# Kernel optimization log

Hardware: AMD Instinct MI355X
Metric: run time of the kernel (lower is better)

Reference implementation:

```python
import jax, jax.numpy as jnp
import numpy as np

EMBED = 1024
HEADS = 16
DEPTH = EMBED // HEADS
FFN_DIM = 4096
EPS = 1e-9


def layer_norm(x, g, b):
    mu = jnp.mean(x, axis=-1, keepdims=True)
    var = jnp.mean(jnp.square(x - mu), axis=-1, keepdims=True)
    return (x - mu) * jax.lax.rsqrt(var + EPS) * g + b


def setup_inputs() -> dict:
    key = jax.random.key(0)
    ks = jax.random.split(key, 16)
    B, S = 2, 2048
    s_e = 1.0 / np.sqrt(EMBED)
    s_f = 1.0 / np.sqrt(FFN_DIM)
    return {
        "x": jax.random.normal(ks[0], (B, S, EMBED), dtype=jnp.float32),
        "mask": jnp.zeros((B, 1, 1, S), dtype=jnp.float32),
        "wq_w": jax.random.normal(ks[1], (EMBED, EMBED), dtype=jnp.float32) * s_e,
        "wq_b": jnp.zeros((EMBED,), dtype=jnp.float32),
        "wk_w": jax.random.normal(ks[2], (EMBED, EMBED), dtype=jnp.float32) * s_e,
        "wk_b": jnp.zeros((EMBED,), dtype=jnp.float32),
        "wv_w": jax.random.normal(ks[3], (EMBED, EMBED), dtype=jnp.float32) * s_e,
        "wv_b": jnp.zeros((EMBED,), dtype=jnp.float32),
        "wo_w": jax.random.normal(ks[4], (EMBED, EMBED), dtype=jnp.float32) * s_e,
        "wo_b": jnp.zeros((EMBED,), dtype=jnp.float32),
        "f1_w": jax.random.normal(ks[5], (EMBED, FFN_DIM), dtype=jnp.float32) * s_e,
        "f1_b": jnp.zeros((FFN_DIM,), dtype=jnp.float32),
        "f2_w": jax.random.normal(ks[6], (FFN_DIM, EMBED), dtype=jnp.float32) * s_f,
        "f2_b": jnp.zeros((EMBED,), dtype=jnp.float32),
        "ln1_g": jnp.ones((EMBED,), dtype=jnp.float32),
        "ln1_b": jnp.zeros((EMBED,), dtype=jnp.float32),
        "ln2_g": jnp.ones((EMBED,), dtype=jnp.float32),
        "ln2_b": jnp.zeros((EMBED,), dtype=jnp.float32),
    }


def reference(x, mask, wq_w, wq_b, wk_w, wk_b, wv_w, wv_b, wo_w, wo_b,
              f1_w, f1_b, f2_w, f2_b, ln1_g, ln1_b, ln2_g, ln2_b):
    B, S, E = x.shape

    def split_heads(t):  # (B,S,E) -> (B,H,S,D)
        return t.reshape(B, S, HEADS, DEPTH).transpose(0, 2, 1, 3)

    q = split_heads(x @ wq_w + wq_b)
    k = split_heads(x @ wk_w + wk_b)
    v = split_heads(x @ wv_w + wv_b)

    logits = jnp.einsum("bhqd,bhkd->bhqk", q, k) / jnp.sqrt(jnp.float32(DEPTH))
    logits = logits + mask * -1e12  # mask broadcast (B,1,1,S)
    attn = jax.nn.softmax(logits, axis=-1)
    out = jnp.einsum("bhqk,bhkd->bhqd", attn, v)
    out = out.transpose(0, 2, 1, 3).reshape(B, S, E)
    out = out @ wo_w + wo_b

    # dropout is identity (is_train=False)
    h = layer_norm(out + x, ln1_g, ln1_b)
    f = jax.nn.relu(h @ f1_w + f1_b) @ f2_w + f2_b
    return layer_norm(f + h, ln2_g, ln2_b)
```

## Files before the change

kernel.cpp:

```cpp
#include <hip/hip_runtime.h>
#include <hip/hip_bf16.h>
#include <stdint.h>

typedef __hip_bfloat16 bf16;
typedef __attribute__((ext_vector_type(8))) short short8;
typedef __attribute__((ext_vector_type(4))) short short4v;
typedef __attribute__((ext_vector_type(4))) float floatx4;

#define E_DIM 1024
#define S_LEN 2048
#define NB    2
#define NH    16
#define HD    64
#define FFN   4096
#define MTOT  4096

__device__ __forceinline__ void gl_lds16(const void* g, void* l) {
  __builtin_amdgcn_global_load_lds(
      (__attribute__((address_space(1))) void*)(g),
      (__attribute__((address_space(3))) void*)(l), 16, 0, 0);
}

__device__ __forceinline__ int fswz_v(int row) { return row & 7; }
__device__ __forceinline__ int fswz_k(int row) {
  return ((row ^ (row >> 3)) & 3) | ((((row >> 3) ^ (row >> 4)) & 1) << 2);
}

__global__ __launch_bounds__(256)
void cvt_bf16(const float* __restrict__ in, bf16* __restrict__ out) {
  const size_t i = ((size_t)blockIdx.x * 256 + threadIdx.x) * 4;
  float4 v = *(const float4*)(in + i);
  out[i + 0] = __float2bfloat16(v.x);
  out[i + 1] = __float2bfloat16(v.y);
  out[i + 2] = __float2bfloat16(v.z);
  out[i + 3] = __float2bfloat16(v.w);
}

__global__ __launch_bounds__(256)
void transpose4(const float* __restrict__ s0, const float* __restrict__ s1,
                const float* __restrict__ s2, const float* __restrict__ s3,
                bf16* __restrict__ d0, bf16* __restrict__ d1,
                bf16* __restrict__ d2, bf16* __restrict__ d3) {
  const int z = blockIdx.z;
  const float* in = (z == 0) ? s0 : (z == 1) ? s1 : (z == 2) ? s2 : s3;
  bf16* out = (z == 0) ? d0 : (z == 1) ? d1 : (z == 2) ? d2 : d3;
  __shared__ float tile[32][33];
  const int tx = threadIdx.x & 31;
  const int ty = threadIdx.x >> 5;
  const int c0 = blockIdx.x * 32;
  const int r0 = blockIdx.y * 32;
#pragma unroll
  for (int j = 0; j < 32; j += 8)
    tile[ty + j][tx] = in[(size_t)(r0 + ty + j) * 1024 + c0 + tx];
  __syncthreads();
#pragma unroll
  for (int j = 0; j < 32; j += 8)
    out[(size_t)(c0 + ty + j) * 1024 + r0 + tx] = __float2bfloat16(tile[tx][ty + j]);
}

__global__ __launch_bounds__(256)
void transpose_cvt(const float* __restrict__ in, bf16* __restrict__ out,
                   int R, int C) {
  __shared__ float tile[32][33];
  const int tx = threadIdx.x & 31;
  const int ty = threadIdx.x >> 5;
  const int c0 = blockIdx.x * 32;
  const int r0 = blockIdx.y * 32;
#pragma unroll
  for (int j = 0; j < 32; j += 8)
    tile[ty + j][tx] = in[(size_t)(r0 + ty + j) * C + c0 + tx];
  __syncthreads();
#pragma unroll
  for (int j = 0; j < 32; j += 8)
    out[(size_t)(c0 + ty + j) * R + r0 + tx] = __float2bfloat16(tile[tx][ty + j]);
}

__global__ __launch_bounds__(256)
void prep_bias(const float* __restrict__ qb, const float* __restrict__ kb,
               const float* __restrict__ vb, float* __restrict__ out) {
  const int i = blockIdx.x * 256 + threadIdx.x;
  float v = (i < 1024) ? qb[i] * 0.125f
                       : ((i < 2048) ? kb[i - 1024] : vb[i - 2048]);
  out[i] = v;
}

__global__ __launch_bounds__(256)
void gemm_bt(const bf16* __restrict__ A, const bf16* __restrict__ B,
             const float* __restrict__ bias, void* __restrict__ Cout,
             int M, int N, int K, int mode) {
  __shared__ alignas(16) bf16 sA[128 * 32];
  __shared__ alignas(16) bf16 sB[128 * 32];
  const int tid   = threadIdx.x;
  const int wave  = tid >> 6;
  const int lane  = tid & 63;
  const int row16 = lane & 15;
  const int quad  = lane >> 4;
  const int m0 = blockIdx.x * 128;
  const int n0 = blockIdx.y * 128;
  const int wm = (wave >> 1) * 64;
  const int wn = (wave & 1) * 64;

  floatx4 acc[4][4];
#pragma unroll
  for (int i = 0; i < 4; i++)
#pragma unroll
    for (int j = 0; j < 4; j++) {
      floatx4 z = {0.f, 0.f, 0.f, 0.f};
      acc[i][j] = z;
    }

  for (int k0 = 0; k0 < K; k0 += 32) {
#pragma unroll
    for (int j = 0; j < 2; ++j) {
      const int chunk = wave * 2 + j;
      const int e = chunk * 512 + lane * 8;
      const int r = e >> 5;
      const int kk = e & 31;
      gl_lds16(A + (size_t)(m0 + r) * K + k0 + kk, sA + chunk * 512);
      gl_lds16(B + (size_t)(n0 + r) * K + k0 + kk, sB + chunk * 512);
    }
    __syncthreads();

    short8 af[4], bfr[4];
#pragma unroll
    for (int i = 0; i < 4; i++) {
      af[i]  = *(const short8*)(sA + (wm + i * 16 + row16) * 32 + quad * 8);
      bfr[i] = *(const short8*)(sB + (wn + i * 16 + row16) * 32 + quad * 8);
    }
#pragma unroll
    for (int mi = 0; mi < 4; mi++)
#pragma unroll
      for (int ni = 0; ni < 4; ni++)
        acc[mi][ni] = __builtin_amdgcn_mfma_f32_16x16x32_bf16(
            af[mi], bfr[ni], acc[mi][ni], 0, 0, 0);
    __syncthreads();
  }

  float bval[4];
#pragma unroll
  for (int ni = 0; ni < 4; ni++) bval[ni] = bias[n0 + wn + ni * 16 + row16];

#pragma unroll
  for (int mi = 0; mi < 4; mi++) {
#pragma unroll
    for (int ni = 0; ni < 4; ni++) {
      const int col = n0 + wn + ni * 16 + row16;
      if (mode == 0) {
#pragma unroll
        for (int r = 0; r < 4; r++) {
          const int row = m0 + wm + mi * 16 + quad * 4 + r;
          ((float*)Cout)[(size_t)row * N + col] = acc[mi][ni][r] + bval[ni];
        }
      } else if (mode == 1) {
#pragma unroll
        for (int r = 0; r < 4; r++) {
          const int row = m0 + wm + mi * 16 + quad * 4 + r;
          float v = acc[mi][ni][r] + bval[ni];
          v = v > 0.f ? v : 0.f;
          ((bf16*)Cout)[(size_t)row * N + col] = __float2bfloat16(v);
        }
      } else {
        const int mat = col >> 10;
        const int c10 = col & 1023;
        const int hh = c10 >> 6, dd = c10 & 63;
        const float scl = (mat == 0) ? 0.125f : 1.0f;
        bf16* qout = (bf16*)Cout;
        const int rbase = m0 + wm + mi * 16 + quad * 4;
        const int b = rbase >> 11, s = rbase & 2047;
        const size_t bh = (size_t)b * NH + hh;
        if (mat == 2) {
          bf16* vt = qout + (1 << 23);
          short4v pv;
#pragma unroll
          for (int r = 0; r < 4; r++) {
            bf16 t = __float2bfloat16(acc[mi][ni][r] + bval[ni]);
            pv[r] = *(short*)&t;
          }
          *(short4v*)(vt + (bh * HD + dd) * S_LEN + s) = pv;
        } else {
          bf16* o = (mat == 1) ? (qout + (1 << 22)) : qout;
#pragma unroll
          for (int r = 0; r < 4; r++) {
            float v = acc[mi][ni][r] * scl + bval[ni];
            o[(bh * S_LEN + s + r) * HD + dd] = __float2bfloat16(v);
          }
        }
      }
    }
  }
}

__global__ __launch_bounds__(256, 4)
void flash_attn(const bf16* __restrict__ Q, const bf16* __restrict__ K,
                const bf16* __restrict__ Vt, const float* __restrict__ mask,
                bf16* __restrict__ Out) {
  __shared__ alignas(16) bf16 sK[64 * 64];
  __shared__ alignas(16) bf16 sV[64 * 64];
  __shared__ alignas(16) float sM[S_LEN];

  const int tid   = threadIdx.x;
  const int wave  = tid >> 6;
  const int lane  = tid & 63;
  const int row16 = lane & 15;
  const int quad  = lane >> 4;
  const int bh = blockIdx.y;
  const int b = bh >> 4, h = bh & 15;
  const int q0 = blockIdx.x * 64;
  const int qg = q0 + wave * 16 + row16;

  const bf16* qp = Q + ((size_t)bh * S_LEN + qg) * HD;
  short8 qf0 = *(const short8*)(qp + quad * 8);
  short8 qf1 = *(const short8*)(qp + 32 + quad * 8);

  for (int i = tid; i < S_LEN / 4; i += 256) {
    float4 mv = ((const float4*)(mask + (size_t)b * S_LEN))[i];
    float4 w = {-1e12f * mv.x, -1e12f * mv.y, -1e12f * mv.z, -1e12f * mv.w};
    ((float4*)sM)[i] = w;
  }

  float m_i = -1e30f, l_i = 0.f;
  floatx4 ov[4];
#pragma unroll
  for (int i = 0; i < 4; i++) { floatx4 z = {0.f,0.f,0.f,0.f}; ov[i] = z; }

  const bf16* Kbase = K + (size_t)bh * S_LEN * HD;
  const bf16* Vbase = Vt + (size_t)bh * HD * S_LEN;

  for (int kt = 0; kt < S_LEN / 64; ++kt) {
    const bf16* Kg = Kbase + (size_t)kt * 64 * HD;
    const bf16* Vg = Vbase + kt * 64;
#pragma unroll
    for (int j = 0; j < 2; ++j) {
      const int ch = wave * 2 + j;
      const int row = ch * 8 + (lane >> 3);
      const int sc_ = lane & 7;
      gl_lds16(Kg + row * 64 + ((sc_ ^ fswz_k(row)) * 8), sK + ch * 512);
      gl_lds16(Vg + (size_t)row * S_LEN + ((sc_ ^ fswz_v(row)) * 8), sV + ch * 512);
    }
    __syncthreads();

    floatx4 sc[4];
#pragma unroll
    for (int mi = 0; mi < 4; mi++) {
      const int row = ((row16 >> 2) << 3) + (row16 & 3) + ((mi & 1) << 2) + ((mi >> 1) << 5);
      const int fk = fswz_k(row);
      short8 kf0 = *(const short8*)(sK + row * 64 + ((quad ^ fk) << 3));
      short8 kf1 = *(const short8*)(sK + row * 64 + (((4 + quad) ^ fk) << 3));
      floatx4 z = {0.f, 0.f, 0.f, 0.f};
      z = __builtin_amdgcn_mfma_f32_16x16x32_bf16(kf0, qf0, z, 0, 0, 0);
      sc[mi] = __builtin_amdgcn_mfma_f32_16x16x32_bf16(kf1, qf1, z, 0, 0, 0);
    }

#pragma unroll
    for (int mi = 0; mi < 4; mi++) {
      float4 mv = *(const float4*)(sM + kt * 64 + (quad << 3) + ((mi & 1) << 2) + ((mi >> 1) << 5));
      sc[mi][0] += mv.x; sc[mi][1] += mv.y; sc[mi][2] += mv.z; sc[mi][3] += mv.w;
    }

    float t = sc[0][0];
#pragma unroll
    for (int mi = 0; mi < 4; mi++)
#pragma unroll
      for (int r = 0; r < 4; r++) t = fmaxf(t, sc[mi][r]);
    t = fmaxf(t, __shfl_xor(t, 16));
    t = fmaxf(t, __shfl_xor(t, 32));
    const float m_new = fmaxf(m_i, t);
    const float alpha = __expf(m_i - m_new);
    m_i = m_new;
    float tsum = 0.f;
#pragma unroll
    for (int mi = 0; mi < 4; mi++)
#pragma unroll
      for (int r = 0; r < 4; r++) {
        float p = __expf(sc[mi][r] - m_new);
        sc[mi][r] = p;
        tsum += p;
      }
    tsum += __shfl_xor(tsum, 16);
    tsum += __shfl_xor(tsum, 32);
    l_i = l_i * alpha + tsum;

    short8 pf[2];
#pragma unroll
    for (int ks = 0; ks < 2; ks++)
#pragma unroll
      for (int jp = 0; jp < 4; jp++) {
        const int mi = 2 * ks + (jp >> 1);
        const int r0 = (jp & 1) * 2;
        bf16 p0 = __float2bfloat16(sc[mi][r0]);
        bf16 p1 = __float2bfloat16(sc[mi][r0 + 1]);
        pf[ks][2 * jp]     = *(short*)&p0;
        pf[ks][2 * jp + 1] = *(short*)&p1;
      }

#pragma unroll
    for (int mi = 0; mi < 4; mi++)
#pragma unroll
      for (int r = 0; r < 4; r++) ov[mi][r] *= alpha;
#pragma unroll
    for (int mi = 0; mi < 4; mi++) {
      const int row = mi * 16 + row16;
      const int fv = fswz_v(row);
      short8 v0 = *(const short8*)(sV + row * 64 + ((quad ^ fv) << 3));
      short8 v1 = *(const short8*)(sV + row * 64 + (((4 + quad) ^ fv) << 3));
      ov[mi] = __builtin_amdgcn_mfma_f32_16x16x32_bf16(v0, pf[0], ov[mi], 0, 0, 0);
      ov[mi] = __builtin_amdgcn_mfma_f32_16x16x32_bf16(v1, pf[1], ov[mi], 0, 0, 0);
    }
    __syncthreads();
  }

  const float inv = 1.0f / l_i;
#pragma unroll
  for (int mi = 0; mi < 4; mi++) {
    short4v pv;
#pragma unroll
    for (int r = 0; r < 4; r++) {
      bf16 t = __float2bfloat16(ov[mi][r] * inv);
      pv[r] = *(short*)&t;
    }
    *(short4v*)(Out + ((size_t)(b * S_LEN + qg)) * E_DIM + h * HD + mi * 16 + quad * 4) = pv;
  }
}

__global__ __launch_bounds__(256)
void ln_fused(const float* __restrict__ A, const float* __restrict__ Bres,
              const float* __restrict__ g, const float* __restrict__ be,
              float* __restrict__ outf, bf16* __restrict__ outb) {
  const int row = blockIdx.x;
  const int tid = threadIdx.x;
  const size_t base = (size_t)row * 1024;
  float4 a = *(const float4*)(A + base + tid * 4);
  float4 b = *(const float4*)(Bres + base + tid * 4);
  float4 xv;
  xv.x = a.x + b.x; xv.y = a.y + b.y; xv.z = a.z + b.z; xv.w = a.w + b.w;
  float s  = xv.x + xv.y + xv.z + xv.w;
  float s2 = xv.x * xv.x + xv.y * xv.y + xv.z * xv.z + xv.w * xv.w;
#pragma unroll
  for (int d = 1; d < 64; d <<= 1) {
    s  += __shfl_xor(s, d);
    s2 += __shfl_xor(s2, d);
  }
  __shared__ float red[2][4];
  const int wave = tid >> 6;
  if ((tid & 63) == 0) { red[0][wave] = s; red[1][wave] = s2; }
  __syncthreads();
  s  = red[0][0] + red[0][1] + red[0][2] + red[0][3];
  s2 = red[1][0] + red[1][1] + red[1][2] + red[1][3];
  const float mu  = s * (1.0f / 1024.0f);
  const float var = s2 * (1.0f / 1024.0f) - mu * mu;
  const float rs  = rsqrtf(var + 1e-9f);
  float4 gg = *(const float4*)(g + tid * 4);
  float4 bb = *(const float4*)(be + tid * 4);
  float4 y;
  y.x = (xv.x - mu) * rs * gg.x + bb.x;
  y.y = (xv.y - mu) * rs * gg.y + bb.y;
  y.z = (xv.z - mu) * rs * gg.z + bb.z;
  y.w = (xv.w - mu) * rs * gg.w + bb.w;
  *(float4*)(outf + base + tid * 4) = y;
  if (outb) {
    bf16* o = outb + base + tid * 4;
    o[0] = __float2bfloat16(y.x);
    o[1] = __float2bfloat16(y.y);
    o[2] = __float2bfloat16(y.z);
    o[3] = __float2bfloat16(y.w);
  }
}

extern "C" void kernel_launch(void* const* d_in, const int* in_sizes, int n_in,
                              void* d_out, int out_size, void* d_ws,
                              size_t ws_size, hipStream_t stream) {
  const float* x    = (const float*)d_in[0];
  const float* mask = (const float*)d_in[1];
  const float* wq_w = (const float*)d_in[2];
  const float* wq_b = (const float*)d_in[3];
  const float* wk_w = (const float*)d_in[4];
  const float* wk_b = (const float*)d_in[5];
  const float* wv_w = (const float*)d_in[6];
  const float* wv_b = (const float*)d_in[7];
  const float* wo_w = (const float*)d_in[8];
  const float* wo_b = (const float*)d_in[9];
  const float* f1_w = (const float*)d_in[10];
  const float* f1_b = (const float*)d_in[11];
  const float* f2_w = (const float*)d_in[12];
  const float* f2_b = (const float*)d_in[13];
  const float* ln1_g = (const float*)d_in[14];
  const float* ln1_b = (const float*)d_in[15];
  const float* ln2_g = (const float*)d_in[16];
  const float* ln2_b = (const float*)d_in[17];
  float* out = (float*)d_out;

  char* ws = (char*)d_ws;
  const size_t MB = 1u << 20;
  bf16*  xbf   = (bf16*)(ws + 0 * MB);
  bf16*  W3T   = (bf16*)(ws + 8 * MB);
  bf16*  woT   = (bf16*)(ws + 14 * MB);
  bf16*  f1T   = (bf16*)(ws + 16 * MB);
  bf16*  f2T   = (bf16*)(ws + 24 * MB);
  float* bqkv  = (float*)(ws + 32 * MB);
  bf16*  Qb    = (bf16*)(ws + 33 * MB);
  bf16*  attnb = (bf16*)(ws + 0 * MB);
  float* proj  = (float*)(ws + 57 * MB);
  float* h     = (float*)(ws + 73 * MB);
  bf16*  hbf   = (bf16*)(ws + 89 * MB);
  bf16*  ffn1  = (bf16*)(ws + 33 * MB);
  float* f2o   = (float*)(ws + 0 * MB);

  cvt_bf16<<<4096, 256, 0, stream>>>(x, xbf);
  transpose4<<<dim3(32, 32, 4), 256, 0, stream>>>(
      wq_w, wk_w, wv_w, wo_w,
      W3T, W3T + 1024 * 1024, W3T + 2 * 1024 * 1024, woT);
  transpose_cvt<<<dim3(128, 32), 256, 0, stream>>>(f1_w, f1T, 1024, 4096);
  transpose_cvt<<<dim3(32, 128), 256, 0, stream>>>(f2_w, f2T, 4096, 1024);
  prep_bias<<<12, 256, 0, stream>>>(wq_b, wk_b, wv_b, bqkv);

  gemm_bt<<<dim3(32, 24), 256, 0, stream>>>(xbf, W3T, bqkv, Qb,
                                            MTOT, 3 * E_DIM, E_DIM, 2);

  flash_attn<<<dim3(S_LEN / 64, NB * NH), 256, 0, stream>>>(
      Qb, Qb + (1 << 22), Qb + (1 << 23), mask, attnb);

  gemm_bt<<<dim3(32, 8), 256, 0, stream>>>(attnb, woT, wo_b, proj,
                                           MTOT, E_DIM, E_DIM, 0);

  ln_fused<<<MTOT, 256, 0, stream>>>(proj, x, ln1_g, ln1_b, h, hbf);

  gemm_bt<<<dim3(32, 32), 256, 0, stream>>>(hbf, f1T, f1_b, ffn1,
                                            MTOT, FFN, E_DIM, 1);
  gemm_bt<<<dim3(32, 8), 256, 0, stream>>>(ffn1, f2T, f2_b, f2o,
                                           MTOT, E_DIM, FFN, 0);

  ln_fused<<<MTOT, 256, 0, stream>>>(f2o, h, ln2_g, ln2_b, out, nullptr);
}
```

Baseline: 436.2 us.

## Split-K the N=1024 GEMMs and fuse partial reduction into layernorm

The output-projection and FFN2 GEMMs are split along K into two partial fp32 buffers, doubling the grid to fill more CUs. The two partials are summed with bias and residual inside a new layernorm kernel. The weight transposes are merged into one launch, and the fp32 copy of h is dropped in favour of the bf16 one as the second residual. In exchange this adds extra partial-buffer traffic and slightly lowers residual precision.

Measured after the change: 391.3 us. 1.11x faster.

```diff
diff --git a/kernel.cpp b/kernel.cpp
--- a/kernel.cpp
+++ b/kernel.cpp
@@ -24,6 +24,12 @@
 __device__ __forceinline__ int fswz_v(int row) { return row & 7; }
 __device__ __forceinline__ int fswz_k(int row) {
   return ((row ^ (row >> 3)) & 3) | ((((row >> 3) ^ (row >> 4)) & 1) << 2);
+}
+
+__device__ __forceinline__ float bf16bits2float(short s) {
+  union { unsigned u; float f; } c;
+  c.u = ((unsigned)(unsigned short)s) << 16;
+  return c.f;
 }
 
 __global__ __launch_bounds__(256)
@@ -37,13 +43,26 @@
 }
 
 __global__ __launch_bounds__(256)
-void transpose4(const float* __restrict__ s0, const float* __restrict__ s1,
-                const float* __restrict__ s2, const float* __restrict__ s3,
-                bf16* __restrict__ d0, bf16* __restrict__ d1,
-                bf16* __restrict__ d2, bf16* __restrict__ d3) {
+void transpose_all(const float* __restrict__ wq, const float* __restrict__ wk,
+                   const float* __restrict__ wv, const float* __restrict__ wo,
+                   const float* __restrict__ f1, const float* __restrict__ f2,
+                   bf16* __restrict__ W3T, bf16* __restrict__ woT,
+                   bf16* __restrict__ f1T, bf16* __restrict__ f2T) {
   const int z = blockIdx.z;
-  const float* in = (z == 0) ? s0 : (z == 1) ? s1 : (z == 2) ? s2 : s3;
-  bf16* out = (z == 0) ? d0 : (z == 1) ? d1 : (z == 2) ? d2 : d3;
+  const float* in;
+  bf16* out;
+  int inStride, outStride, rOff, cOff;
+  if (z < 4) {
+    in = (z == 0) ? wq : (z == 1) ? wk : (z == 2) ? wv : wo;
+    out = (z < 3) ? (W3T + (size_t)z * 1024 * 1024) : woT;
+    inStride = 1024; outStride = 1024; rOff = 0; cOff = 0;
+  } else if (z < 8) {
+    in = f1; out = f1T; inStride = 4096; outStride = 1024;
+    rOff = 0; cOff = (z - 4) * 1024;
+  } else {
+    in = f2; out = f2T; inStride = 1024; outStride = 4096;
+    rOff = (z - 8) * 1024; cOff = 0;
+  }
   __shared__ float tile[32][33];
   const int tx = threadIdx.x & 31;
   const int ty = threadIdx.x >> 5;
@@ -51,28 +70,13 @@
   const int r0 = blockIdx.y * 32;
 #pragma unroll
   for (int j = 0; j < 32; j += 8)
-    tile[ty + j][tx] = in[(size_t)(r0 + ty + j) * 1024 + c0 + tx];
+    tile[ty + j][tx] =
+        in[(size_t)(rOff + r0 + ty + j) * inStride + cOff + c0 + tx];
   __syncthreads();
 #pragma unroll
   for (int j = 0; j < 32; j += 8)
-    out[(size_t)(c0 + ty + j) * 1024 + r0 + tx] = __float2bfloat16(tile[tx][ty + j]);
-}
-
-__global__ __launch_bounds__(256)
-void transpose_cvt(const float* __restrict__ in, bf16* __restrict__ out,
-                   int R, int C) {
-  __shared__ float tile[32][33];
-  const int tx = threadIdx.x & 31;
-  const int ty = threadIdx.x >> 5;
-  const int c0 = blockIdx.x * 32;
-  const int r0 = blockIdx.y * 32;
-#pragma unroll
-  for (int j = 0; j < 32; j += 8)
-    tile[ty + j][tx] = in[(size_t)(r0 + ty + j) * C + c0 + tx];
-  __syncthreads();
-#pragma unroll
-  for (int j = 0; j < 32; j += 8)
-    out[(size_t)(c0 + ty + j) * R + r0 + tx] = __float2bfloat16(tile[tx][ty + j]);
+    out[(size_t)(cOff + c0 + ty + j) * outStride + rOff + r0 + tx] =
+        __float2bfloat16(tile[tx][ty + j]);
 }
 
 __global__ __launch_bounds__(256)
@@ -87,7 +91,7 @@
 __global__ __launch_bounds__(256)
 void gemm_bt(const bf16* __restrict__ A, const bf16* __restrict__ B,
              const float* __restrict__ bias, void* __restrict__ Cout,
-             int M, int N, int K, int mode) {
+             int M, int N, int Kpart, int lda, int mode) {
   __shared__ alignas(16) bf16 sA[128 * 32];
   __shared__ alignas(16) bf16 sB[128 * 32];
   const int tid   = threadIdx.x;
@@ -99,6 +103,7 @@
   const int n0 = blockIdx.y * 128;
   const int wm = (wave >> 1) * 64;
   const int wn = (wave & 1) * 64;
+  const int koff = blockIdx.z * Kpart;
 
   floatx4 acc[4][4];
 #pragma unroll
@@ -109,15 +114,15 @@
       acc[i][j] = z;
     }
 
-  for (int k0 = 0; k0 < K; k0 += 32) {
+  for (int k0 = koff; k0 < koff + Kpart; k0 += 32) {
 #pragma unroll
     for (int j = 0; j < 2; ++j) {
       const int chunk = wave * 2 + j;
       const int e = chunk * 512 + lane * 8;
       const int r = e >> 5;
       const int kk = e & 31;
-      gl_lds16(A + (size_t)(m0 + r) * K + k0 + kk, sA + chunk * 512);
-      gl_lds16(B + (size_t)(n0 + r) * K + k0 + kk, sB + chunk * 512);
+      gl_lds16(A + (size_t)(m0 + r) * lda + k0 + kk, sA + chunk * 512);
+      gl_lds16(B + (size_t)(n0 + r) * lda + k0 + kk, sB + chunk * 512);
     }
     __syncthreads();
 
@@ -136,9 +141,11 @@
     __syncthreads();
   }
 
-  float bval[4];
-#pragma unroll
-  for (int ni = 0; ni < 4; ni++) bval[ni] = bias[n0 + wn + ni * 16 + row16];
+  float bval[4] = {0.f, 0.f, 0.f, 0.f};
+  if (mode != 0) {
+#pragma unroll
+    for (int ni = 0; ni < 4; ni++) bval[ni] = bias[n0 + wn + ni * 16 + row16];
+  }
 
 #pragma unroll
   for (int mi = 0; mi < 4; mi++) {
@@ -146,10 +153,11 @@
     for (int ni = 0; ni < 4; ni++) {
       const int col = n0 + wn + ni * 16 + row16;
       if (mode == 0) {
+        float* co = (float*)Cout + (size_t)blockIdx.z * M * N;
 #pragma unroll
         for (int r = 0; r < 4; r++) {
           const int row = m0 + wm + mi * 16 + quad * 4 + r;
-          ((float*)Cout)[(size_t)row * N + col] = acc[mi][ni][r] + bval[ni];
+          co[(size_t)row * N + col] = acc[mi][ni][r];
         }
       } else if (mode == 1) {
 #pragma unroll
@@ -323,16 +331,33 @@
 }
 
 __global__ __launch_bounds__(256)
-void ln_fused(const float* __restrict__ A, const float* __restrict__ Bres,
-              const float* __restrict__ g, const float* __restrict__ be,
-              float* __restrict__ outf, bf16* __restrict__ outb) {
+void ln_reduce(const float* __restrict__ p0, const float* __restrict__ p1,
+               const float* __restrict__ resf, const bf16* __restrict__ resb,
+               const float* __restrict__ bias, const float* __restrict__ g,
+               const float* __restrict__ be, float* __restrict__ outf,
+               bf16* __restrict__ outb) {
   const int row = blockIdx.x;
   const int tid = threadIdx.x;
   const size_t base = (size_t)row * 1024;
-  float4 a = *(const float4*)(A + base + tid * 4);
-  float4 b = *(const float4*)(Bres + base + tid * 4);
+  const int c = tid * 4;
+  float4 a = *(const float4*)(p0 + base + c);
+  float4 bq = *(const float4*)(p1 + base + c);
+  float4 rv;
+  if (resf) {
+    rv = *(const float4*)(resf + base + c);
+  } else {
+    short4v rb = *(const short4v*)((const short*)resb + base + c);
+    rv.x = bf16bits2float(rb[0]);
+    rv.y = bf16bits2float(rb[1]);
+    rv.z = bf16bits2float(rb[2]);
+    rv.w = bf16bits2float(rb[3]);
+  }
+  float4 bi = *(const float4*)(bias + c);
   float4 xv;
-  xv.x = a.x + b.x; xv.y = a.y + b.y; xv.z = a.z + b.z; xv.w = a.w + b.w;
+  xv.x = a.x + bq.x + rv.x + bi.x;
+  xv.y = a.y + bq.y + rv.y + bi.y;
+  xv.z = a.z + bq.z + rv.z + bi.z;
+  xv.w = a.w + bq.w + rv.w + bi.w;
   float s  = xv.x + xv.y + xv.z + xv.w;
   float s2 = xv.x * xv.x + xv.y * xv.y + xv.z * xv.z + xv.w * xv.w;
 #pragma unroll
@@ -349,16 +374,16 @@
   const float mu  = s * (1.0f / 1024.0f);
   const float var = s2 * (1.0f / 1024.0f) - mu * mu;
   const float rs  = rsqrtf(var + 1e-9f);
-  float4 gg = *(const float4*)(g + tid * 4);
-  float4 bb = *(const float4*)(be + tid * 4);
+  float4 gg = *(const float4*)(g + c);
+  float4 bb = *(const float4*)(be + c);
   float4 y;
   y.x = (xv.x - mu) * rs * gg.x + bb.x;
   y.y = (xv.y - mu) * rs * gg.y + bb.y;
   y.z = (xv.z - mu) * rs * gg.z + bb.z;
   y.w = (xv.w - mu) * rs * gg.w + bb.w;
-  *(float4*)(outf + base + tid * 4) = y;
+  if (outf) *(float4*)(outf + base + c) = y;
   if (outb) {
-    bf16* o = outb + base + tid * 4;
+    bf16* o = outb + base + c;
     o[0] = __float2bfloat16(y.x);
     o[1] = __float2bfloat16(y.y);
     o[2] = __float2bfloat16(y.z);
@@ -394,40 +419,39 @@
   bf16*  xbf   = (bf16*)(ws + 0 * MB);
   bf16*  W3T   = (bf16*)(ws + 8 * MB);
   bf16*  woT   = (bf16*)(ws + 14 * MB);
-  bf16*  f1T   = (bf16*)(ws + 16 * MB);
-  bf16*  f2T   = (bf16*)(ws + 24 * MB);
-  float* bqkv  = (float*)(ws + 32 * MB);
-  bf16*  Qb    = (bf16*)(ws + 33 * MB);
+  float* bqkv  = (float*)(ws + 16 * MB);
+  bf16*  Qb    = (bf16*)(ws + 17 * MB);
   bf16*  attnb = (bf16*)(ws + 0 * MB);
-  float* proj  = (float*)(ws + 57 * MB);
-  float* h     = (float*)(ws + 73 * MB);
-  bf16*  hbf   = (bf16*)(ws + 89 * MB);
-  bf16*  ffn1  = (bf16*)(ws + 33 * MB);
-  float* f2o   = (float*)(ws + 0 * MB);
+  bf16*  ffn1  = (bf16*)(ws + 17 * MB);
+  bf16*  f1T   = (bf16*)(ws + 49 * MB);
+  bf16*  f2T   = (bf16*)(ws + 57 * MB);
+  float* parts = (float*)(ws + 65 * MB);
+  bf16*  hbf   = (bf16*)(ws + 97 * MB);
+  const size_t PSTRIDE = (size_t)MTOT * E_DIM;
 
   cvt_bf16<<<4096, 256, 0, stream>>>(x, xbf);
-  transpose4<<<dim3(32, 32, 4), 256, 0, stream>>>(
-      wq_w, wk_w, wv_w, wo_w,
-      W3T, W3T + 1024 * 1024, W3T + 2 * 1024 * 1024, woT);
-  transpose_cvt<<<dim3(128, 32), 256, 0, stream>>>(f1_w, f1T, 1024, 4096);
-  transpose_cvt<<<dim3(32, 128), 256, 0, stream>>>(f2_w, f2T, 4096, 1024);
+  transpose_all<<<dim3(32, 32, 12), 256, 0, stream>>>(
+      wq_w, wk_w, wv_w, wo_w, f1_w, f2_w, W3T, woT, f1T, f2T);
   prep_bias<<<12, 256, 0, stream>>>(wq_b, wk_b, wv_b, bqkv);
 
-  gemm_bt<<<dim3(32, 24), 256, 0, stream>>>(xbf, W3T, bqkv, Qb,
-                                            MTOT, 3 * E_DIM, E_DIM, 2);
+  gemm_bt<<<dim3(32, 24, 1), 256, 0, stream>>>(xbf, W3T, bqkv, Qb,
+                                               MTOT, 3 * E_DIM, E_DIM, E_DIM, 2);
 
   flash_attn<<<dim3(S_LEN / 64, NB * NH), 256, 0, stream>>>(
       Qb, Qb + (1 << 22), Qb + (1 << 23), mask, attnb);
 
-  gemm_bt<<<dim3(32, 8), 256, 0, stream>>>(attnb, woT, wo_b, proj,
-                                           MTOT, E_DIM, E_DIM, 0);
-
-  ln_fused<<<MTOT, 256, 0, stream>>>(proj, x, ln1_g, ln1_b, h, hbf);
-
-  gemm_bt<<<dim3(32, 32), 256, 0, stream>>>(hbf, f1T, f1_b, ffn1,
-                                            MTOT, FFN, E_DIM, 1);
-  gemm_bt<<<dim3(32, 8), 256, 0, stream>>>(ffn1, f2T, f2_b, f2o,
-                                           MTOT, E_DIM, FFN, 0);
-
-  ln_fused<<<MTOT, 256, 0, stream>>>(f2o, h, ln2_g, ln2_b, out, nullptr);
-}
+  gemm_bt<<<dim3(32, 8, 2), 256, 0, stream>>>(attnb, woT, nullptr, parts,
+                                              MTOT, E_DIM, E_DIM / 2, E_DIM, 0);
+
+  ln_reduce<<<MTOT, 256, 0, stream>>>(parts, parts + PSTRIDE, x, nullptr,
+                                      wo_b, ln1_g, ln1_b, nullptr, hbf);
+
+  gemm_bt<<<dim3(32, 32, 1), 256, 0, stream>>>(hbf, f1T, f1_b, ffn1,
+                                               MTOT, FFN, E_DIM, E_DIM, 1);
+
+  gemm_bt<<<dim3(32, 8, 2), 256, 0, stream>>>(ffn1, f2T, nullptr, parts,
+                                              MTOT, E_DIM, FFN / 2, FFN, 0);
+
+  ln_reduce<<<MTOT, 256, 0, stream>>>(parts, parts + PSTRIDE, nullptr, hbf,
+                                      f2_b, ln2_g, ln2_b, out, nullptr);
+}
```
